# Kernel optimization log

Hardware: AMD Instinct MI355X
Metric: run time of the kernel (lower is better)

## Reference

```python
import jax, jax.numpy as jnp
import numpy as np

CAPACITY_FACTOR = 2  # GShard top-2 gating: C = 2*S/E


def setup_inputs() -> dict:
    key = jax.random.key(0)
    k1, k2, k3, k4 = jax.random.split(key, 4)
    B, T, M, E, F = 4, 1024, 1024, 8, 4096
    x = jax.random.normal(k1, (B, T, M), dtype=jnp.float32)
    wg = jax.random.normal(k2, (M, E), dtype=jnp.float32) * 0.02
    w1 = jax.random.normal(k3, (E, M, F), dtype=jnp.float32) * 0.02
    w2 = jax.random.normal(k4, (E, F, M), dtype=jnp.float32) * 0.02
    return {"x": x, "wg": wg, "w1": w1, "w2": w2}


def top2_gate(xs, wg):
    # xs: [S, M] tokens; wg: [M, E] gate projection.
    S = xs.shape[0]
    E = wg.shape[1]
    C = CAPACITY_FACTOR * S // E  # expert capacity
    logits = xs @ wg                                  # [S, E]
    gates = jax.nn.softmax(logits, axis=-1)           # [S, E]
    # top-1 expert
    idx1 = jnp.argmax(gates, axis=-1)                 # [S]
    mask1 = jax.nn.one_hot(idx1, E, dtype=jnp.int32)  # [S, E]
    # top-2 expert: mask out top-1 and take argmax again
    logits_no1 = jnp.where(mask1.astype(bool), -jnp.inf, logits)
    idx2 = jnp.argmax(logits_no1, axis=-1)
    mask2 = jax.nn.one_hot(idx2, E, dtype=jnp.int32)
    # positions within each expert's buffer (cumsum over tokens)
    loc1 = jnp.cumsum(mask1, axis=0) - 1              # [S, E]
    loc2 = jnp.cumsum(mask2, axis=0) - 1 + jnp.sum(mask1, axis=0, keepdims=True)
    # load-balancing auxiliary loss
    me = jnp.mean(gates, axis=0)
    ce = jnp.mean(mask1.astype(gates.dtype), axis=0)
    l_aux = jnp.mean(me * ce) * (E * E)
    # drop tokens beyond capacity
    mask1 = mask1 * (loc1 < C)
    mask2 = mask2 * (loc2 < C)
    loc1_s = jnp.sum(loc1 * mask1, axis=1)            # [S] slot of token in its top-1 expert
    loc2_s = jnp.sum(loc2 * mask2, axis=1)
    mask1f = mask1.astype(gates.dtype)
    mask2f = mask2.astype(gates.dtype)
    gates1_s = jnp.sum(gates * mask1f, axis=1)
    gates2_s = jnp.sum(gates * mask2f, axis=1)
    denom = gates1_s + gates2_s
    denom = jnp.where(denom < 1e-9, 1e-9, denom)
    g1 = gates1_s / denom
    g2 = gates2_s / denom
    # combine weights [S, E, C]
    combine = (g1[:, None] * mask1f)[:, :, None] * jax.nn.one_hot(loc1_s, C, dtype=gates.dtype)[:, None, :] \
            + (g2[:, None] * mask2f)[:, :, None] * jax.nn.one_hot(loc2_s, C, dtype=gates.dtype)[:, None, :]
    dispatch = (combine > 0).astype(gates.dtype)      # one-hot dispatch mask [S, E, C]
    return l_aux, combine, dispatch


def reference(x, wg, w1, w2):
    B, T, M = x.shape
    xs = x.reshape(-1, M)                                  # [S, M]
    l_aux, combine_weights, dispatch_mask = top2_gate(xs, wg)
    # dispatch: one-hot matmul (E*C x S) @ (S x M) -> [E, C, M]
    dispatched = jnp.einsum('sec,sm->ecm', dispatch_mask, xs)
    # per-expert FFN (relu)
    h = jax.nn.relu(jnp.einsum('ecm,emf->ecf', dispatched, w1))
    expert_out = jnp.einsum('ecf,efm->ecm', h, w2)         # [E, C, M]
    # combine: (S x E*C) @ (E*C x M) -> [S, M]
    combined = jnp.einsum('sec,ecm->sm', combine_weights, expert_out)
    return combined.reshape(B, T, M), l_aux
```

## Files before the change

### kernel.cpp

```cpp
#include <hip/hip_runtime.h>
#include <hip/hip_bf16.h>

typedef unsigned short u16;
typedef short bf16x8 __attribute__((ext_vector_type(8)));
typedef float f32x4 __attribute__((ext_vector_type(4)));
typedef u16 u16x8 __attribute__((ext_vector_type(8)));

#define S_TOK 4096
#define MDIM 1024
#define EDIM 8
#define FDIM 4096
#define CCAP 1024
#define HALF_F 2048

__device__ __align__(16) u16   g_xb [S_TOK * MDIM];
__device__ __align__(16) u16   g_wT [EDIM * FDIM * MDIM];
__device__ __align__(16) u16   g_h  [EDIM * CCAP * FDIM];
__device__ __align__(16) float g_eo [2 * EDIM * CCAP * MDIM];
__device__ float g_gates[S_TOK * EDIM];
__device__ int   g_idx1[S_TOK], g_idx2[S_TOK];
__device__ int   g_loc1[S_TOK], g_loc2[S_TOK];
__device__ float g_tg1[S_TOK],  g_tg2[S_TOK];
__device__ int   g_ts1[S_TOK],  g_ts2[S_TOK];
__device__ int   g_slot[EDIM * CCAP];

__device__ __forceinline__ u16 f2bf(float f) {
    union { float f; unsigned u; } c; c.f = f;
    unsigned r = c.u + 0x7FFFu + ((c.u >> 16) & 1u);
    return (u16)(r >> 16);
}
__device__ __forceinline__ void async16(const void* g, void* l) {
    __builtin_amdgcn_global_load_lds(
        (const __attribute__((address_space(1))) unsigned int*)g,
        (__attribute__((address_space(3))) unsigned int*)l, 16, 0, 0);
}

__global__ void cvt_x(const float* __restrict__ x) {
    int i = (blockIdx.x * 256 + threadIdx.x) * 8;
    float4 a = *(const float4*)(x + i);
    float4 b = *(const float4*)(x + i + 4);
    u16x8 o;
    o[0] = f2bf(a.x); o[1] = f2bf(a.y); o[2] = f2bf(a.z); o[3] = f2bf(a.w);
    o[4] = f2bf(b.x); o[5] = f2bf(b.y); o[6] = f2bf(b.z); o[7] = f2bf(b.w);
    *(u16x8*)(g_xb + i) = o;
}

__global__ void gate_kernel(const float* __restrict__ x, const float* __restrict__ wg) {
    __shared__ float wgT[EDIM * MDIM];
    const int tid = threadIdx.x, wave = tid >> 6, lane = tid & 63;
    for (int i = tid; i < EDIM * MDIM; i += 256) {
        int e = i >> 10, m = i & 1023;
        wgT[i] = wg[m * EDIM + e];
    }
    __syncthreads();
    const int s = blockIdx.x * 4 + wave;
    const float* xr = x + (size_t)s * MDIM;
    float lg[EDIM];
#pragma unroll
    for (int e = 0; e < EDIM; e++) lg[e] = 0.f;
#pragma unroll
    for (int j = 0; j < 4; j++) {
        int m0 = j * 256 + lane * 4;
        float4 xv = *(const float4*)(xr + m0);
#pragma unroll
        for (int e = 0; e < EDIM; e++) {
            float4 wv = *(const float4*)(&wgT[e * MDIM + m0]);
            lg[e] += xv.x * wv.x + xv.y * wv.y + xv.z * wv.z + xv.w * wv.w;
        }
    }
#pragma unroll
    for (int e = 0; e < EDIM; e++) {
        float v = lg[e];
        for (int o = 32; o >= 1; o >>= 1) v += __shfl_xor(v, o);
        lg[e] = v;
    }
    if (lane == 0) {
        float mx = lg[0];
#pragma unroll
        for (int e = 1; e < EDIM; e++) mx = fmaxf(mx, lg[e]);
        float ex[EDIM], sum = 0.f;
#pragma unroll
        for (int e = 0; e < EDIM; e++) { ex[e] = expf(lg[e] - mx); sum += ex[e]; }
        int i1 = 0; float b1 = lg[0];
#pragma unroll
        for (int e = 1; e < EDIM; e++) if (lg[e] > b1) { b1 = lg[e]; i1 = e; }
        int i2 = -1; float b2 = -3.4e38f;
#pragma unroll
        for (int e = 0; e < EDIM; e++) if (e != i1 && lg[e] > b2) { b2 = lg[e]; i2 = e; }
        float inv = 1.f / sum;
#pragma unroll
        for (int e = 0; e < EDIM; e++) g_gates[s * EDIM + e] = ex[e] * inv;
        g_idx1[s] = i1; g_idx2[s] = i2;
    }
}

__global__ void scan_kernel(float* __restrict__ out_laux) {
    __shared__ float me_sh[EDIM];
    __shared__ int cnt_sh[EDIM];
    const int t = threadIdx.x, wave = t >> 6, lane = t & 63;
    if (t < EDIM) { me_sh[t] = 0.f; cnt_sh[t] = 0; }
    for (int i = t; i < EDIM * CCAP; i += 1024) g_slot[i] = -1;
    __syncthreads();
    float lm[EDIM]; int lc[EDIM];
#pragma unroll
    for (int e = 0; e < EDIM; e++) { lm[e] = 0.f; lc[e] = 0; }
    for (int j = 0; j < 4; j++) {
        int s = t + 1024 * j;
        const float* g = g_gates + (size_t)s * EDIM;
        int i1 = g_idx1[s];
#pragma unroll
        for (int e = 0; e < EDIM; e++) { lm[e] += g[e]; lc[e] += (i1 == e); }
    }
#pragma unroll
    for (int e = 0; e < EDIM; e++) {
        float v = lm[e]; int c = lc[e];
        for (int o = 32; o >= 1; o >>= 1) { v += __shfl_xor(v, o); c += __shfl_xor(c, o); }
        if (lane == 0) { atomicAdd(&me_sh[e], v); atomicAdd(&cnt_sh[e], c); }
    }
    __syncthreads();
    {
        int e = wave & 7;
        const int* idx = (wave < 8) ? g_idx1 : g_idx2;
        int* loc = (wave < 8) ? g_loc1 : g_loc2;
        int running = (wave < 8) ? 0 : cnt_sh[e];
        for (int s0 = 0; s0 < S_TOK; s0 += 64) {
            int v = idx[s0 + lane];
            bool f = (v == e);
            unsigned long long m = __ballot(f);
            int rank = __popcll(m & ((1ull << lane) - 1ull));
            if (f) loc[s0 + lane] = running + rank;
            running += __popcll(m);
        }
    }
    __syncthreads();
    for (int j = 0; j < 4; j++) {
        int s = t + 1024 * j;
        int e1 = g_idx1[s], e2 = g_idx2[s];
        int l1 = g_loc1[s], l2 = g_loc2[s];
        bool k1 = l1 < CCAP, k2 = l2 < CCAP;
        float G1 = k1 ? g_gates[s * EDIM + e1] : 0.f;
        float G2 = k2 ? g_gates[s * EDIM + e2] : 0.f;
        float den = G1 + G2; den = den < 1e-9f ? 1e-9f : den;
        g_tg1[s] = G1 / den; g_tg2[s] = G2 / den;
        g_ts1[s] = k1 ? (e1 * CCAP + l1) : -1;
        g_ts2[s] = k2 ? (e2 * CCAP + l2) : -1;
        if (k1) g_slot[e1 * CCAP + l1] = s;
        if (k2) g_slot[e2 * CCAP + l2] = s;
    }
    if (t == 0) {
        float la = 0.f;
        for (int e = 0; e < EDIM; e++)
            la += (me_sh[e] / (float)S_TOK) * ((float)cnt_sh[e] / (float)S_TOK);
        la *= (float)EDIM;
        out_laux[0] = la;
    }
}

template <int R, int C>
__global__ void transpose_cvt(const float* __restrict__ in) {
    __shared__ __align__(16) u16 t[64][72];
    const float* I = in + (size_t)blockIdx.z * R * C;
    u16* O = g_wT + (size_t)blockIdx.z * R * C;
    const int tid = threadIdx.x;
    const int c0 = blockIdx.x * 64, r0 = blockIdx.y * 64;
    const int rr = tid >> 4;
    const int cc = (tid & 15) * 4;
#pragma unroll
    for (int j = 0; j < 4; j++) {
        int r = rr + j * 16;
        float4 v = *(const float4*)(I + (size_t)(r0 + r) * C + c0 + cc);
        t[cc + 0][r] = f2bf(v.x);
        t[cc + 1][r] = f2bf(v.y);
        t[cc + 2][r] = f2bf(v.z);
        t[cc + 3][r] = f2bf(v.w);
    }
    __syncthreads();
    const int oc = tid >> 2;
    const int orr = (tid & 3) * 16;
    u16x8 a = *(const u16x8*)(&t[oc][orr]);
    u16x8 b = *(const u16x8*)(&t[oc][orr + 8]);
    u16* dst = O + (size_t)(c0 + oc) * R + r0 + orr;
    *(u16x8*)(dst) = a;
    *(u16x8*)(dst + 8) = b;
}

#define GSTAGE(sA, sB)                                                      \
    {                                                                       \
        async16(gA0, sA + stA0); async16(gA1, sA + stA1);                   \
        async16(gB0, sB + stA0); async16(gB1, sB + stA1);                   \
        gA0 += 32; gA1 += 32; gB0 += 32; gB1 += 32;                         \
    }

#define GCOMPUTE(sA, sB)                                                    \
    {                                                                       \
        bf16x8 af[4], bfr[4];                                               \
        _Pragma("unroll")                                                   \
        for (int i = 0; i < 4; i++) {                                       \
            af[i]  = *(const bf16x8*)(sA + (wm + i * 16 + lrow) * 32 + cr); \
            bfr[i] = *(const bf16x8*)(sB + (wn + i * 16 + lrow) * 32 + cr); \
        }                                                                   \
        __builtin_amdgcn_s_setprio(1);                                      \
        _Pragma("unroll")                                                   \
        for (int mi = 0; mi < 4; mi++)                                      \
            _Pragma("unroll")                                               \
            for (int ni = 0; ni < 4; ni++)                                  \
                acc[mi][ni] = __builtin_amdgcn_mfma_f32_16x16x32_bf16(      \
                    af[mi], bfr[ni], acc[mi][ni], 0, 0, 0);                 \
        __builtin_amdgcn_s_setprio(0);                                      \
    }

#define WAIT4 asm volatile("s_waitcnt vmcnt(4)" ::: "memory")
#define WAIT0 asm volatile("s_waitcnt vmcnt(0)" ::: "memory")
#define BAR   __builtin_amdgcn_s_barrier()

#define GEMM_PIPELINE(T)                                                    \
    GSTAGE(As0, Bs0);                                                       \
    GSTAGE(As1, Bs1);                                                       \
    for (int t = 0; t < (T) - 2; t += 2) {                                  \
        WAIT4; BAR;                                                         \
        GCOMPUTE(As0, Bs0);                                                 \
        BAR;                                                                \
        GSTAGE(As0, Bs0);                                                   \
        WAIT4; BAR;                                                         \
        GCOMPUTE(As1, Bs1);                                                 \
        BAR;                                                                \
        GSTAGE(As1, Bs1);                                                   \
    }                                                                       \
    WAIT4; BAR;                                                             \
    GCOMPUTE(As0, Bs0);                                                     \
    WAIT0; BAR;                                                             \
    GCOMPUTE(As1, Bs1);

__global__ __launch_bounds__(256, 4) void gemm_gather() {
    __shared__ __align__(16) u16 As0[4096], As1[4096], Bs0[4096], Bs1[4096];
    const int tid = threadIdx.x, wave = tid >> 6, lane = tid & 63;
    const int id = (blockIdx.x & 7) * 256 + (blockIdx.x >> 3);
    const int by = id & 7, bx = (id >> 3) & 31, e = id >> 8;
    const int scol = (((lane & 3) ^ ((lane >> 3) & 3)) * 8);
    const int stA0 = wave * 512, stA1 = 2048 + wave * 512;
    const int sb = e * CCAP + by * 128;
    int s0 = g_slot[sb + wave * 16 + (lane >> 2)];      if (s0 < 0) s0 = 0;
    int s1 = g_slot[sb + 64 + wave * 16 + (lane >> 2)]; if (s1 < 0) s1 = 0;
    const u16* gA0 = g_xb + (size_t)s0 * MDIM + scol;
    const u16* gA1 = g_xb + (size_t)s1 * MDIM + scol;
    const u16* Bb = g_wT + ((size_t)e * FDIM + bx * 128) * MDIM;
    const u16* gB0 = Bb + (size_t)(wave * 16 + (lane >> 2)) * MDIM + scol;
    const u16* gB1 = gB0 + (size_t)64 * MDIM;

    f32x4 acc[4][4];
#pragma unroll
    for (int i = 0; i < 4; i++)
#pragma unroll
        for (int j = 0; j < 4; j++) { f32x4 z = {0.f, 0.f, 0.f, 0.f}; acc[i][j] = z; }
    const int wm = (wave >> 1) * 64, wn = (wave & 1) * 64;
    const int lrow = lane & 15, lq = lane >> 4;
    const int cr = ((lq ^ ((lrow >> 1) & 3)) * 8);

    GEMM_PIPELINE(MDIM / 32)

    const int r0 = by * 128 + wm + lq * 4;
    const int c0 = bx * 128 + wn + lrow;
    u16* D = g_h + (size_t)e * CCAP * FDIM;
#pragma unroll
    for (int mi = 0; mi < 4; mi++)
#pragma unroll
        for (int v = 0; v < 4; v++) {
            size_t r = (size_t)(r0 + mi * 16 + v) * FDIM;
#pragma unroll
            for (int ni = 0; ni < 4; ni++) {
                float xv = acc[mi][ni][v];
                xv = xv > 0.f ? xv : 0.f;
                D[r + c0 + ni * 16] = f2bf(xv);
            }
        }
}

__global__ __launch_bounds__(256, 4) void gemm_bt() {
    __shared__ __align__(16) u16 As0[4096], As1[4096], Bs0[4096], Bs1[4096];
    const int tid = threadIdx.x, wave = tid >> 6, lane = tid & 63;
    const int id = (blockIdx.x & 7) * 128 + (blockIdx.x >> 3);
    const int by = id & 7, bx = (id >> 3) & 7, z = id >> 6;
    const int e = z >> 1, ks = z & 1;
    const int scol = (((lane & 3) ^ ((lane >> 3) & 3)) * 8);
    const int stA0 = wave * 512, stA1 = 2048 + wave * 512;
    const u16* Ab = g_h + (size_t)e * CCAP * FDIM + (size_t)(by * 128) * FDIM + ks * HALF_F;
    const u16* Bb = g_wT + (size_t)e * MDIM * FDIM + (size_t)(bx * 128) * FDIM + ks * HALF_F;
    const u16* gA0 = Ab + (size_t)(wave * 16 + (lane >> 2)) * FDIM + scol;
    const u16* gA1 = gA0 + (size_t)64 * FDIM;
    const u16* gB0 = Bb + (size_t)(wave * 16 + (lane >> 2)) * FDIM + scol;
    const u16* gB1 = gB0 + (size_t)64 * FDIM;

    f32x4 acc[4][4];
#pragma unroll
    for (int i = 0; i < 4; i++)
#pragma unroll
        for (int j = 0; j < 4; j++) { f32x4 z2 = {0.f, 0.f, 0.f, 0.f}; acc[i][j] = z2; }
    const int wm = (wave >> 1) * 64, wn = (wave & 1) * 64;
    const int lrow = lane & 15, lq = lane >> 4;
    const int cr = ((lq ^ ((lrow >> 1) & 3)) * 8);

    GEMM_PIPELINE(HALF_F / 32)

    const int r0 = by * 128 + wm + lq * 4;
    const int c0 = bx * 128 + wn + lrow;
    float* D = g_eo + (size_t)ks * (EDIM * CCAP * MDIM) + (size_t)e * CCAP * MDIM;
#pragma unroll
    for (int mi = 0; mi < 4; mi++)
#pragma unroll
        for (int v = 0; v < 4; v++) {
            size_t r = (size_t)(r0 + mi * 16 + v) * MDIM;
#pragma unroll
            for (int ni = 0; ni < 4; ni++)
                D[r + c0 + ni * 16] = acc[mi][ni][v];
        }
}

__global__ void combine_kernel(float* __restrict__ out) {
    const int s = blockIdx.x, t = threadIdx.x;
    constexpr size_t HALF = (size_t)EDIM * CCAP * MDIM;
    float g1 = g_tg1[s], g2 = g_tg2[s];
    int p1 = g_ts1[s], p2 = g_ts2[s];
    float a0 = 0.f, a1 = 0.f, a2 = 0.f, a3 = 0.f;
    if (p1 >= 0) {
        float4 v = ((const float4*)(g_eo + (size_t)p1 * MDIM))[t];
        float4 w = ((const float4*)(g_eo + HALF + (size_t)p1 * MDIM))[t];
        a0 = g1 * (v.x + w.x); a1 = g1 * (v.y + w.y);
        a2 = g1 * (v.z + w.z); a3 = g1 * (v.w + w.w);
    }
    if (p2 >= 0) {
        float4 v = ((const float4*)(g_eo + (size_t)p2 * MDIM))[t];
        float4 w = ((const float4*)(g_eo + HALF + (size_t)p2 * MDIM))[t];
        a0 += g2 * (v.x + w.x); a1 += g2 * (v.y + w.y);
        a2 += g2 * (v.z + w.z); a3 += g2 * (v.w + w.w);
    }
    float4 o; o.x = a0; o.y = a1; o.z = a2; o.w = a3;
    ((float4*)out)[(size_t)s * 256 + t] = o;
}

extern "C" void kernel_launch(void* const* d_in, const int* in_sizes, int n_in,
                              void* d_out, int out_size, void* d_ws, size_t ws_size,
                              hipStream_t stream) {
    const float* x  = (const float*)d_in[0];
    const float* wg = (const float*)d_in[1];
    const float* w1 = (const float*)d_in[2];
    const float* w2 = (const float*)d_in[3];
    float* out = (float*)d_out;

    cvt_x<<<dim3(S_TOK * MDIM / 2048), 256, 0, stream>>>(x);
    gate_kernel<<<dim3(S_TOK / 4), 256, 0, stream>>>(x, wg);
    scan_kernel<<<dim3(1), 1024, 0, stream>>>(out + 4194304);

    transpose_cvt<MDIM, FDIM><<<dim3(FDIM / 64, MDIM / 64, EDIM), 256, 0, stream>>>(w1);
    gemm_gather<<<dim3(2048), 256, 0, stream>>>();

    transpose_cvt<FDIM, MDIM><<<dim3(MDIM / 64, FDIM / 64, EDIM), 256, 0, stream>>>(w2);
    gemm_bt<<<dim3(1024), 256, 0, stream>>>();

    combine_kernel<<<dim3(S_TOK), 256, 0, stream>>>(out);
}
```

Baseline: 537.3 us.

## Triple-buffer GEMM LDS pipeline and fuse x bf16 conversion into gate kernel

Moves both expert GEMMs from a two-stage to a three-stage LDS ring (rotating pointers, vmcnt(8) waits), so two tiles of global loads are in flight during each compute step. Occupancy is lowered to 3 blocks per CU to fit the larger shared memory. Separately, the standalone x-to-bf16 conversion kernel is removed and the conversion is done inside the gate kernel, which already reads x, saving one launch and one pass over x. The risks are lower occupancy and a per-iteration branch on the wait count in the now non-unrolled loop.

Result: no change. 540.8 us (+0.7%).

```diff
diff --git a/kernel.cpp b/kernel.cpp
--- a/kernel.cpp
+++ b/kernel.cpp
@@ -5,6 +5,7 @@
 typedef short bf16x8 __attribute__((ext_vector_type(8)));
 typedef float f32x4 __attribute__((ext_vector_type(4)));
 typedef u16 u16x8 __attribute__((ext_vector_type(8)));
+typedef u16 u16x4 __attribute__((ext_vector_type(4)));
 
 #define S_TOK 4096
 #define MDIM 1024
@@ -35,16 +36,6 @@
         (__attribute__((address_space(3))) unsigned int*)l, 16, 0, 0);
 }
 
-__global__ void cvt_x(const float* __restrict__ x) {
-    int i = (blockIdx.x * 256 + threadIdx.x) * 8;
-    float4 a = *(const float4*)(x + i);
-    float4 b = *(const float4*)(x + i + 4);
-    u16x8 o;
-    o[0] = f2bf(a.x); o[1] = f2bf(a.y); o[2] = f2bf(a.z); o[3] = f2bf(a.w);
-    o[4] = f2bf(b.x); o[5] = f2bf(b.y); o[6] = f2bf(b.z); o[7] = f2bf(b.w);
-    *(u16x8*)(g_xb + i) = o;
-}
-
 __global__ void gate_kernel(const float* __restrict__ x, const float* __restrict__ wg) {
     __shared__ float wgT[EDIM * MDIM];
     const int tid = threadIdx.x, wave = tid >> 6, lane = tid & 63;
@@ -62,6 +53,9 @@
     for (int j = 0; j < 4; j++) {
         int m0 = j * 256 + lane * 4;
         float4 xv = *(const float4*)(xr + m0);
+        u16x4 xb;
+        xb[0] = f2bf(xv.x); xb[1] = f2bf(xv.y); xb[2] = f2bf(xv.z); xb[3] = f2bf(xv.w);
+        *(u16x4*)(g_xb + (size_t)s * MDIM + m0) = xb;
 #pragma unroll
         for (int e = 0; e < EDIM; e++) {
             float4 wv = *(const float4*)(&wgT[e * MDIM + m0]);
@@ -184,20 +178,20 @@
     *(u16x8*)(dst + 8) = b;
 }
 
-#define GSTAGE(sA, sB)                                                      \
+#define GSTAGE(pA, pB)                                                      \
     {                                                                       \
-        async16(gA0, sA + stA0); async16(gA1, sA + stA1);                   \
-        async16(gB0, sB + stA0); async16(gB1, sB + stA1);                   \
+        async16(gA0, (pA) + stA0); async16(gA1, (pA) + stA1);               \
+        async16(gB0, (pB) + stA0); async16(gB1, (pB) + stA1);               \
         gA0 += 32; gA1 += 32; gB0 += 32; gB1 += 32;                         \
     }
 
-#define GCOMPUTE(sA, sB)                                                    \
+#define GCOMPUTE(pA, pB)                                                    \
     {                                                                       \
         bf16x8 af[4], bfr[4];                                               \
         _Pragma("unroll")                                                   \
         for (int i = 0; i < 4; i++) {                                       \
-            af[i]  = *(const bf16x8*)(sA + (wm + i * 16 + lrow) * 32 + cr); \
-            bfr[i] = *(const bf16x8*)(sB + (wn + i * 16 + lrow) * 32 + cr); \
+            af[i]  = *(const bf16x8*)((pA) + (wm + i * 16 + lrow) * 32 + cr);\
+            bfr[i] = *(const bf16x8*)((pB) + (wn + i * 16 + lrow) * 32 + cr);\
         }                                                                   \
         __builtin_amdgcn_s_setprio(1);                                      \
         _Pragma("unroll")                                                   \
@@ -209,30 +203,27 @@
         __builtin_amdgcn_s_setprio(0);                                      \
     }
 
-#define WAIT4 asm volatile("s_waitcnt vmcnt(4)" ::: "memory")
-#define WAIT0 asm volatile("s_waitcnt vmcnt(0)" ::: "memory")
-#define BAR   __builtin_amdgcn_s_barrier()
+#define BAR __builtin_amdgcn_s_barrier()
 
 #define GEMM_PIPELINE(T)                                                    \
-    GSTAGE(As0, Bs0);                                                       \
-    GSTAGE(As1, Bs1);                                                       \
-    for (int t = 0; t < (T) - 2; t += 2) {                                  \
-        WAIT4; BAR;                                                         \
-        GCOMPUTE(As0, Bs0);                                                 \
+    u16 *pa0 = As0, *pa1 = As1, *pa2 = As2;                                 \
+    u16 *pb0 = Bs0, *pb1 = Bs1, *pb2 = Bs2;                                 \
+    GSTAGE(pa0, pb0); GSTAGE(pa1, pb1); GSTAGE(pa2, pb2);                   \
+    for (int t = 0; t < (T); ++t) {                                         \
+        if (t < (T) - 2)       { asm volatile("s_waitcnt vmcnt(8)" ::: "memory"); } \
+        else if (t == (T) - 2) { asm volatile("s_waitcnt vmcnt(4)" ::: "memory"); } \
+        else                   { asm volatile("s_waitcnt vmcnt(0)" ::: "memory"); } \
         BAR;                                                                \
-        GSTAGE(As0, Bs0);                                                   \
-        WAIT4; BAR;                                                         \
-        GCOMPUTE(As1, Bs1);                                                 \
+        GCOMPUTE(pa0, pb0);                                                 \
         BAR;                                                                \
-        GSTAGE(As1, Bs1);                                                   \
-    }                                                                       \
-    WAIT4; BAR;                                                             \
-    GCOMPUTE(As0, Bs0);                                                     \
-    WAIT0; BAR;                                                             \
-    GCOMPUTE(As1, Bs1);
-
-__global__ __launch_bounds__(256, 4) void gemm_gather() {
-    __shared__ __align__(16) u16 As0[4096], As1[4096], Bs0[4096], Bs1[4096];
+        if (t + 3 < (T)) { GSTAGE(pa0, pb0); }                              \
+        u16* tA = pa0; pa0 = pa1; pa1 = pa2; pa2 = tA;                      \
+        u16* tB = pb0; pb0 = pb1; pb1 = pb2; pb2 = tB;                      \
+    }
+
+__global__ __launch_bounds__(256, 3) void gemm_gather() {
+    __shared__ __align__(16) u16 As0[4096], As1[4096], As2[4096];
+    __shared__ __align__(16) u16 Bs0[4096], Bs1[4096], Bs2[4096];
     const int tid = threadIdx.x, wave = tid >> 6, lane = tid & 63;
     const int id = (blockIdx.x & 7) * 256 + (blockIdx.x >> 3);
     const int by = id & 7, bx = (id >> 3) & 31, e = id >> 8;
@@ -275,8 +266,9 @@
         }
 }
 
-__global__ __launch_bounds__(256, 4) void gemm_bt() {
-    __shared__ __align__(16) u16 As0[4096], As1[4096], Bs0[4096], Bs1[4096];
+__global__ __launch_bounds__(256, 3) void gemm_bt() {
+    __shared__ __align__(16) u16 As0[4096], As1[4096], As2[4096];
+    __shared__ __align__(16) u16 Bs0[4096], Bs1[4096], Bs2[4096];
     const int tid = threadIdx.x, wave = tid >> 6, lane = tid & 63;
     const int id = (blockIdx.x & 7) * 128 + (blockIdx.x >> 3);
     const int by = id & 7, bx = (id >> 3) & 7, z = id >> 6;
@@ -346,7 +338,6 @@
     const float* w2 = (const float*)d_in[3];
     float* out = (float*)d_out;
 
-    cvt_x<<<dim3(S_TOK * MDIM / 2048), 256, 0, stream>>>(x);
     gate_kernel<<<dim3(S_TOK / 4), 256, 0, stream>>>(x, wg);
     scan_kernel<<<dim3(1), 1024, 0, stream>>>(out + 4194304);
 
```
